# Kernel optimization log

Measured on AMD Instinct MI355X. Metric: run time of the kernel, lower is better.

## Reference

```python
import jax, jax.numpy as jnp
import numpy as np

E, H, W = 1024, 16, 256  # embed_dim, num_heads, window_size
D = E // H               # head_dim


def _rmsnorm(t, w):
    eps = jnp.finfo(t.dtype).eps
    return t * jax.lax.rsqrt(jnp.mean(t * t, axis=-1, keepdims=True) + eps) * w


def setup_inputs() -> dict:
    key = jax.random.key(0)
    ks = jax.random.split(key, 11)
    B, T = 2, 2048
    s = 1.0 / np.sqrt(E)
    return {
        "x": jax.random.normal(ks[0], (B, T, E), jnp.float32),
        "wq": jax.random.normal(ks[1], (E, E), jnp.float32) * s,
        "bq": jnp.zeros((E,), jnp.float32),
        "wk": jax.random.normal(ks[2], (E, E), jnp.float32) * s,
        "bk": jnp.zeros((E,), jnp.float32),
        "wv": jax.random.normal(ks[3], (E, E), jnp.float32) * s,
        "bv": jnp.zeros((E,), jnp.float32),
        "wo": jax.random.normal(ks[4], (E, E), jnp.float32) * s,
        "bo": jnp.zeros((E,), jnp.float32),
        "qn_w": jnp.ones((D,), jnp.float32),
        "kn_w": jnp.ones((D,), jnp.float32),
    }


def reference(x, wq, bq, wk, bk, wv, bv, wo, bo, qn_w, kn_w):
    B, T, _ = x.shape
    # projections; weights stored (in, out)
    q = (x @ wq + bq).reshape(B, T, H, D).transpose(0, 2, 1, 3)  # [B,H,T,D]
    k = (x @ wk + bk).reshape(B, T, H, D).transpose(0, 2, 1, 3)
    v = (x @ wv + bv).reshape(B, T, H, D).transpose(0, 2, 1, 3)
    q = _rmsnorm(q, qn_w)
    k = _rmsnorm(k, kn_w)

    scores = jnp.einsum("bhqd,bhkd->bhqk", q, k) / jnp.sqrt(jnp.float32(D))
    row = jnp.arange(T)[:, None]
    col = jnp.arange(T)[None, :]
    invalid = (col > row) | (row - col >= W)  # causal + sliding window
    neg_inf = jnp.float32(-jnp.inf)
    scores = jnp.where(invalid, neg_inf, scores)

    # genetic fitness reweighting
    masked_attn = jnp.where(invalid, 0.0, jax.nn.softmax(scores, axis=-1))
    gene_means = jnp.mean(jax.nn.sigmoid(masked_attn), axis=-1)  # [B,H,T]
    denom = gene_means + 0.5
    sum_inv = jnp.sum(1.0 / denom, axis=2, keepdims=True)        # [B,H,1]
    fitness = 1.0 / (denom * sum_inv)                            # [B,H,T]
    scores = scores + jnp.log(fitness)[..., None]

    attn = jax.nn.softmax(scores, axis=-1)
    out = jnp.einsum("bhqk,bhkd->bhqd", attn, v)
    out = out.transpose(0, 2, 1, 3).reshape(B, T, E)
    return out @ wo + bo
```

## Files before the change

kernel.cpp:

```cpp
#include <hip/hip_runtime.h>

typedef _Float16 f16;
typedef _Float16 f16x4 __attribute__((ext_vector_type(4)));
typedef _Float16 f16x8 __attribute__((ext_vector_type(8)));
typedef float f32x4 __attribute__((ext_vector_type(4)));

#define MFMA16(a, b, c) __builtin_amdgcn_mfma_f32_16x16x32_f16(a, b, c, 0, 0, 0)

constexpr int T = 2048;
constexpr int E = 1024;
constexpr int H = 16;
constexpr int D = 64;
constexpr int WIN = 256;
#define NEGF (-1e30f)
#define L2E 1.4426950408889634f

__device__ __forceinline__ void gload16(const f16* g, f16* l) {
  __builtin_amdgcn_global_load_lds(
      (__attribute__((address_space(1))) void*)(void*)g,
      (__attribute__((address_space(3))) void*)(void*)l, 16, 0, 0);
}

__global__ __launch_bounds__(256) void cast_x_kernel(const float* __restrict__ x,
                                                     f16* __restrict__ xb) {
  int idx = (blockIdx.x * 256 + threadIdx.x) * 4;
  float4 v = *(const float4*)(x + idx);
  f16x4 o = {(f16)v.x, (f16)v.y, (f16)v.z, (f16)v.w};
  *(f16x4*)(xb + idx) = o;
}

__global__ __launch_bounds__(256) void transpose_w_kernel(
    const float* __restrict__ w0, const float* __restrict__ w1,
    const float* __restrict__ w2, const float* __restrict__ w3,
    f16* __restrict__ o0, f16* __restrict__ o1, f16* __restrict__ o2,
    f16* __restrict__ o3) {
  int z = blockIdx.z;
  const float* w = z == 0 ? w0 : z == 1 ? w1 : z == 2 ? w2 : w3;
  f16* o = z == 0 ? o0 : z == 1 ? o1 : z == 2 ? o2 : o3;
  __shared__ float tile[64][65];
  int k0 = blockIdx.x * 64, n0 = blockIdx.y * 64;
  int r = threadIdx.x >> 2, cb = (threadIdx.x & 3) * 16;
  const float* src = w + (size_t)(k0 + r) * E + n0 + cb;
#pragma unroll
  for (int j = 0; j < 16; j += 4) {
    float4 v = *(const float4*)(src + j);
    tile[r][cb + j] = v.x;
    tile[r][cb + j + 1] = v.y;
    tile[r][cb + j + 2] = v.z;
    tile[r][cb + j + 3] = v.w;
  }
  __syncthreads();
  f16 tmp[16];
#pragma unroll
  for (int j = 0; j < 16; ++j) tmp[j] = (f16)tile[cb + j][r];
  f16* dst = o + (size_t)(n0 + r) * E + k0 + cb;
  *(f16x8*)dst = *(f16x8*)&tmp[0];
  *(f16x8*)(dst + 8) = *(f16x8*)&tmp[8];
}

__global__ __launch_bounds__(256) void qkv_fused_kernel(
    const f16* __restrict__ A, const f16* __restrict__ Bq,
    const f16* __restrict__ Bk, const f16* __restrict__ Bv,
    const float* __restrict__ cq, const float* __restrict__ ck,
    const float* __restrict__ cv, const float* __restrict__ qnw,
    const float* __restrict__ knw, f16* __restrict__ oq, f16* __restrict__ ok,
    f16* __restrict__ Vt) {
  const int K = E, N = E;
  __shared__ f16 lA[2][8192];
  __shared__ f16 lB[3][2][8192];

  int m0 = blockIdx.x * 128, n0 = blockIdx.y * 128;
  int tid = threadIdx.x;
  int wid = tid >> 6, lane = tid & 63;
  int wm = wid >> 1, wn = wid & 1;
  int lr = lane & 15, lg = lane >> 4;

  f32x4 zero = {0.f, 0.f, 0.f, 0.f};
  f32x4 acc[3][4][4];
#pragma unroll
  for (int z = 0; z < 3; ++z)
    for (int a = 0; a < 4; ++a)
      for (int b = 0; b < 4; ++b) acc[z][a][b] = zero;

  int srow = lane >> 3;
  int scol = (lane & 7) << 3;

  auto stage = [&](int buf, int k0) {
#pragma unroll
    for (int p = 0; p < 4; ++p) {
      int cc = (wid << 2) + p;
      int row = (cc << 3) + srow;
      int gc = scol ^ ((row & 7) << 3);
      size_t ga = (size_t)(m0 + row) * K + k0 + gc;
      size_t gb = (size_t)(n0 + row) * K + k0 + gc;
      gload16(A + ga, &lA[buf][cc << 9]);
      gload16(Bq + gb, &lB[0][buf][cc << 9]);
      gload16(Bk + gb, &lB[1][buf][cc << 9]);
      gload16(Bv + gb, &lB[2][buf][cc << 9]);
    }
  };

  stage(0, 0);
  __syncthreads();
  int cur = 0;
  for (int t = 0; t < 16; ++t) {
    if (t + 1 < 16) stage(cur ^ 1, (t + 1) << 6);
#pragma unroll
    for (int kk = 0; kk < 2; ++kk) {
      int kc = kk * 32 + (lg << 3);
      f16x8 af[4];
#pragma unroll
      for (int mt = 0; mt < 4; ++mt) {
        int row = wm * 64 + mt * 16 + lr;
        af[mt] = *(const f16x8*)&lA[cur][((row << 6) + kc) ^ ((row & 7) << 3)];
      }
#pragma unroll
      for (int z = 0; z < 3; ++z) {
#pragma unroll
        for (int nt = 0; nt < 4; ++nt) {
          int row = wn * 64 + nt * 16 + lr;
          f16x8 bf =
              *(const f16x8*)&lB[z][cur][((row << 6) + kc) ^ ((row & 7) << 3)];
#pragma unroll
          for (int mt = 0; mt < 4; ++mt)
            acc[z][mt][nt] = MFMA16(af[mt], bf, acc[z][mt][nt]);
        }
      }
    }
    if (t + 1 < 16) {
      __syncthreads();
      cur ^= 1;
    }
  }

  const float eps = 1.1920929e-7f;
#pragma unroll
  for (int z = 0; z < 2; ++z) {
    const float* nw = z == 0 ? qnw : knw;
    const float* bias = z == 0 ? cq : ck;
    f16* o = z == 0 ? oq : ok;
    const float osc = z == 0 ? 0.125f : 1.0f;
    float wv_[4];
#pragma unroll
    for (int nt = 0; nt < 4; ++nt) wv_[nt] = nw[nt * 16 + lr] * osc;
#pragma unroll
    for (int mt = 0; mt < 4; ++mt) {
      float vbuf[4][4];
      float ss[4] = {0.f, 0.f, 0.f, 0.f};
#pragma unroll
      for (int nt = 0; nt < 4; ++nt) {
        float bv = bias[n0 + wn * 64 + nt * 16 + lr];
#pragma unroll
        for (int i = 0; i < 4; ++i) {
          float v = acc[z][mt][nt][i] + bv;
          vbuf[nt][i] = v;
          ss[i] += v * v;
        }
      }
      float rr[4];
#pragma unroll
      for (int i = 0; i < 4; ++i) {
        ss[i] += __shfl_xor(ss[i], 1);
        ss[i] += __shfl_xor(ss[i], 2);
        ss[i] += __shfl_xor(ss[i], 4);
        ss[i] += __shfl_xor(ss[i], 8);
        rr[i] = rsqrtf(ss[i] * (1.0f / 64.0f) + eps);
      }
      int row = m0 + wm * 64 + mt * 16 + (lg << 2);
#pragma unroll
      for (int nt = 0; nt < 4; ++nt) {
        int col = n0 + wn * 64 + nt * 16 + lr;
#pragma unroll
        for (int i = 0; i < 4; ++i)
          o[(size_t)(row + i) * N + col] = (f16)(vbuf[nt][i] * rr[i] * wv_[nt]);
      }
    }
  }
#pragma unroll
  for (int mt = 0; mt < 4; ++mt) {
    int row = m0 + wm * 64 + mt * 16 + (lg << 2);
    int b = row >> 11;
    int t = row & (T - 1);
#pragma unroll
    for (int nt = 0; nt < 4; ++nt) {
      int col = n0 + wn * 64 + nt * 16 + lr;
      float bv = cv[col];
      int h = col >> 6, d = col & 63;
      f16x4 pk = {(f16)(acc[2][mt][nt][0] + bv), (f16)(acc[2][mt][nt][1] + bv),
                  (f16)(acc[2][mt][nt][2] + bv), (f16)(acc[2][mt][nt][3] + bv)};
      *(f16x4*)&Vt[(((size_t)(b * H + h) * D + d) << 11) + t] = pk;
    }
  }
}

__global__ __launch_bounds__(256) void out_gemm_kernel(
    const f16* __restrict__ A, const f16* __restrict__ Bt,
    const float* __restrict__ bias, float* __restrict__ out, int M, int N,
    int K) {
  __shared__ f16 lA[2][8192];
  __shared__ f16 lB[2][8192];

  int m0 = blockIdx.x * 128, n0 = blockIdx.y * 128;
  int tid = threadIdx.x;
  int wid = tid >> 6, lane = tid & 63;
  int wm = wid >> 1, wn = wid & 1;
  int lr = lane & 15, lg = lane >> 4;

  f32x4 zero = {0.f, 0.f, 0.f, 0.f};
  f32x4 acc[4][4];
  for (int a = 0; a < 4; ++a)
    for (int b = 0; b < 4; ++b) acc[a][b] = zero;

  int srow = lane >> 3;
  int scol = (lane & 7) << 3;

  auto stage = [&](int buf, int k0) {
#pragma unroll
    for (int p = 0; p < 4; ++p) {
      int cc = (wid << 2) + p;
      int row = (cc << 3) + srow;
      int gc = scol ^ ((row & 7) << 3);
      gload16(A + (size_t)(m0 + row) * K + k0 + gc, &lA[buf][cc << 9]);
      gload16(Bt + (size_t)(n0 + row) * K + k0 + gc, &lB[buf][cc << 9]);
    }
  };

  int nit = K >> 6;
  stage(0, 0);
  __syncthreads();
  int cur = 0;
  for (int t = 0; t < nit; ++t) {
    if (t + 1 < nit) stage(cur ^ 1, (t + 1) << 6);
#pragma unroll
    for (int kk = 0; kk < 2; ++kk) {
      int kc = kk * 32 + (lg << 3);
      f16x8 af[4], bf[4];
#pragma unroll
      for (int mt = 0; mt < 4; ++mt) {
        int row = wm * 64 + mt * 16 + lr;
        af[mt] = *(const f16x8*)&lA[cur][((row << 6) + kc) ^ ((row & 7) << 3)];
      }
#pragma unroll
      for (int nt = 0; nt < 4; ++nt) {
        int row = wn * 64 + nt * 16 + lr;
        bf[nt] = *(const f16x8*)&lB[cur][((row << 6) + kc) ^ ((row & 7) << 3)];
      }
#pragma unroll
      for (int mt = 0; mt < 4; ++mt)
#pragma unroll
        for (int nt = 0; nt < 4; ++nt)
          acc[mt][nt] = MFMA16(af[mt], bf[nt], acc[mt][nt]);
    }
    if (t + 1 < nit) {
      __syncthreads();
      cur ^= 1;
    }
  }

#pragma unroll
  for (int mt = 0; mt < 4; ++mt) {
#pragma unroll
    for (int nt = 0; nt < 4; ++nt) {
      int row = m0 + wm * 64 + mt * 16 + (lg << 2);
      int col = n0 + wn * 64 + nt * 16 + lr;
      float bv = bias[col];
#pragma unroll
      for (int i = 0; i < 4; ++i)
        out[(size_t)(row + i) * N + col] = acc[mt][nt][i] + bv;
    }
  }
}

__global__ __launch_bounds__(256) void attn_kernel(const f16* __restrict__ qn,
                                                   const f16* __restrict__ kn,
                                                   const f16* __restrict__ Vt,
                                                   f16* __restrict__ aout) {
  int q0 = blockIdx.x * 64;
  int bh = blockIdx.y;
  int b = bh >> 4, h = bh & 15;
  int tid = threadIdx.x;
  int w = tid >> 6, lane = tid & 63;
  int lr = lane & 15, lg = lane >> 4;

  __shared__ f16 lK[2][4096];
  __shared__ f16 lV[2][4096];
  __shared__ f16 lP[4096];

  const f16* Qb = qn + (size_t)(b * T + q0 + w * 16 + lr) * E + h * 64 + (lg << 3);
  f16x8 qf0 = *(const f16x8*)Qb;
  f16x8 qf1 = *(const f16x8*)(Qb + 32);

  f32x4 zero = {0.f, 0.f, 0.f, 0.f};
  f32x4 acc[4] = {zero, zero, zero, zero};
  float m[4] = {NEGF, NEGF, NEGF, NEGF};
  float l[4] = {0.f, 0.f, 0.f, 0.f};

  int mi = q0 >> 6;
  int kts = mi - 4 < 0 ? 0 : mi - 4;

  const f16* Kbase = kn + (size_t)b * T * E + h * 64;
  const f16* Vbase = Vt + (size_t)bh * D * T;

  int srow = lane >> 3;
  int scol = (lane & 7) << 3;

  auto stageKV = [&](int buf, int kt) {
    int k0 = kt << 6;
#pragma unroll
    for (int p = 0; p < 2; ++p) {
      int cc = (w << 1) + p;
      int row = (cc << 3) + srow;
      int gc = scol ^ ((row & 7) << 3);
      gload16(Kbase + (size_t)(k0 + row) * E + gc, &lK[buf][cc << 9]);
      gload16(Vbase + (size_t)row * T + k0 + gc, &lV[buf][cc << 9]);
    }
  };

  stageKV(0, kts);
  __syncthreads();
  int cur = 0;

  for (int kt = kts; kt <= mi; ++kt) {
    if (kt < mi) stageKV(cur ^ 1, kt + 1);
    int k0 = kt << 6;

    f32x4 s[4];
#pragma unroll
    for (int ct = 0; ct < 4; ++ct) s[ct] = zero;
#pragma unroll
    for (int kk = 0; kk < 2; ++kk) {
      int kc = kk * 32 + (lg << 3);
#pragma unroll
      for (int ct = 0; ct < 4; ++ct) {
        int row = ct * 16 + lr;
        f16x8 bf = *(const f16x8*)&lK[cur][((row << 6) + kc) ^ ((row & 7) << 3)];
        s[ct] = MFMA16(kk == 0 ? qf0 : qf1, bf, s[ct]);
      }
    }

    float tm[4] = {NEGF, NEGF, NEGF, NEGF};
    int rowg0 = q0 + w * 16 + (lg << 2);
    bool needmask = (kt == mi) || (mi >= 4 && kt == kts);
    if (needmask) {
#pragma unroll
      for (int ct = 0; ct < 4; ++ct) {
        int col = k0 + ct * 16 + lr;
#pragma unroll
        for (int i = 0; i < 4; ++i) {
          int rowg = rowg0 + i;
          float v = s[ct][i];
          if (col > rowg || rowg - col >= WIN) v = NEGF;
          s[ct][i] = v;
          tm[i] = fmaxf(tm[i], v);
        }
      }
    } else {
#pragma unroll
      for (int ct = 0; ct < 4; ++ct)
#pragma unroll
        for (int i = 0; i < 4; ++i) tm[i] = fmaxf(tm[i], s[ct][i]);
    }
#pragma unroll
    for (int i = 0; i < 4; ++i) {
      tm[i] = fmaxf(tm[i], __shfl_xor(tm[i], 1));
      tm[i] = fmaxf(tm[i], __shfl_xor(tm[i], 2));
      tm[i] = fmaxf(tm[i], __shfl_xor(tm[i], 4));
      tm[i] = fmaxf(tm[i], __shfl_xor(tm[i], 8));
    }
    bool up = (tm[0] > m[0]) || (tm[1] > m[1]) || (tm[2] > m[2]) ||
              (tm[3] > m[3]);
    if (__any(up)) {
      float fac[4];
#pragma unroll
      for (int i = 0; i < 4; ++i) {
        float mn = fmaxf(m[i], tm[i]);
        fac[i] = exp2f((m[i] - mn) * L2E);
        m[i] = mn;
        l[i] *= fac[i];
      }
#pragma unroll
      for (int dt = 0; dt < 4; ++dt)
#pragma unroll
        for (int i = 0; i < 4; ++i) acc[dt][i] *= fac[i];
    }
    float ps[4] = {0.f, 0.f, 0.f, 0.f};
#pragma unroll
    for (int ct = 0; ct < 4; ++ct)
#pragma unroll
      for (int i = 0; i < 4; ++i) {
        float p = exp2f((s[ct][i] - m[i]) * L2E);
        s[ct][i] = p;
        ps[i] += p;
      }
#pragma unroll
    for (int i = 0; i < 4; ++i) {
      ps[i] += __shfl_xor(ps[i], 1);
      ps[i] += __shfl_xor(ps[i], 2);
      ps[i] += __shfl_xor(ps[i], 4);
      ps[i] += __shfl_xor(ps[i], 8);
      l[i] += ps[i];
    }

#pragma unroll
    for (int ct = 0; ct < 4; ++ct)
#pragma unroll
      for (int i = 0; i < 4; ++i) {
        int qloc = (lg << 2) + i;
        int el = (qloc << 6) + ct * 16 + lr;
        lP[w * 1024 + (el ^ ((qloc & 7) << 3))] = (f16)s[ct][i];
      }

#pragma unroll
    for (int kk = 0; kk < 2; ++kk) {
      int kc = kk * 32 + (lg << 3);
      int ep = w * 1024 + (((lr << 6) + kc) ^ ((lr & 7) << 3));
      f16x8 pf = *(const f16x8*)&lP[ep];
#pragma unroll
      for (int dt = 0; dt < 4; ++dt) {
        int row = dt * 16 + lr;
        f16x8 vf = *(const f16x8*)&lV[cur][((row << 6) + kc) ^ ((row & 7) << 3)];
        acc[dt] = MFMA16(pf, vf, acc[dt]);
      }
    }

    if (kt < mi) {
      __syncthreads();
      cur ^= 1;
    }
  }

#pragma unroll
  for (int i = 0; i < 4; ++i) {
    float inv = 1.0f / l[i];
    int tok = q0 + w * 16 + (lg << 2) + i;
    f16* dst = aout + (size_t)(b * T + tok) * E + h * 64 + lr;
#pragma unroll
    for (int dt = 0; dt < 4; ++dt) dst[dt * 16] = (f16)(acc[dt][i] * inv);
  }
}

extern "C" void kernel_launch(void* const* d_in, const int* in_sizes, int n_in,
                              void* d_out, int out_size, void* d_ws,
                              size_t ws_size, hipStream_t stream) {
  const float* x = (const float*)d_in[0];
  const float* wq = (const float*)d_in[1];
  const float* bq = (const float*)d_in[2];
  const float* wk = (const float*)d_in[3];
  const float* bk = (const float*)d_in[4];
  const float* wv = (const float*)d_in[5];
  const float* bv = (const float*)d_in[6];
  const float* wo = (const float*)d_in[7];
  const float* bo = (const float*)d_in[8];
  const float* qn_w = (const float*)d_in[9];
  const float* kn_w = (const float*)d_in[10];
  float* out = (float*)d_out;

  char* ws = (char*)d_ws;
  const size_t MB = 1u << 20;
  f16* xb = (f16*)(ws);
  f16* wqT = (f16*)(ws + 8 * MB);
  f16* wkT = (f16*)(ws + 10 * MB);
  f16* wvT = (f16*)(ws + 12 * MB);
  f16* woT = (f16*)(ws + 14 * MB);
  f16* qn = (f16*)(ws + 16 * MB);
  f16* kn = (f16*)(ws + 24 * MB);
  f16* Vt = (f16*)(ws + 32 * MB);
  f16* aout = (f16*)(ws + 40 * MB);

  cast_x_kernel<<<4096, 256, 0, stream>>>(x, xb);
  transpose_w_kernel<<<dim3(16, 16, 4), 256, 0, stream>>>(wq, wk, wv, wo, wqT,
                                                          wkT, wvT, woT);
  qkv_fused_kernel<<<dim3(32, 8), 256, 0, stream>>>(
      xb, wqT, wkT, wvT, bq, bk, bv, qn_w, kn_w, qn, kn, Vt);
  attn_kernel<<<dim3(32, 32), 256, 0, stream>>>(qn, kn, Vt, aout);
  out_gemm_kernel<<<dim3(32, 8), 256, 0, stream>>>(aout, woT, bo, out, 4096,
                                                   1024, 1024);
}
```

Baseline: 107.7 us.

## Restructure QKV GEMM into 256x256 tiles over concatenated weights with split-phase pipeline

Replaces the fused QKV kernel, which computed q, k and v for a 128x128 tile, with a 512-thread kernel that computes one 256x256 output tile of the concatenated QKV weight matrix. Each block now produces only q, k or v, and the grid becomes 16x12 (192 blocks) instead of 256. The K loop is split into two half-steps with staggered A/B loads, manual waitcnt and barriers, and setprio around the MFMA bursts, so that loads overlap with compute. This aims to raise arithmetic intensity per LDS byte and cut pipeline stalls, at the cost of fewer blocks than CUs and more register pressure.

```diff
diff --git a/kernel.cpp b/kernel.cpp
--- a/kernel.cpp
+++ b/kernel.cpp
@@ -58,84 +58,120 @@
   *(f16x8*)(dst + 8) = *(f16x8*)&tmp[8];
 }
 
-__global__ __launch_bounds__(256) void qkv_fused_kernel(
-    const f16* __restrict__ A, const f16* __restrict__ Bq,
-    const f16* __restrict__ Bk, const f16* __restrict__ Bv,
+__global__ __launch_bounds__(512) void qkv256_kernel(
+    const f16* __restrict__ A, const f16* __restrict__ Ball,
     const float* __restrict__ cq, const float* __restrict__ ck,
     const float* __restrict__ cv, const float* __restrict__ qnw,
     const float* __restrict__ knw, f16* __restrict__ oq, f16* __restrict__ ok,
     f16* __restrict__ Vt) {
-  const int K = E, N = E;
-  __shared__ f16 lA[2][8192];
-  __shared__ f16 lB[3][2][8192];
-
-  int m0 = blockIdx.x * 128, n0 = blockIdx.y * 128;
+  const int K = E;
+  __shared__ f16 lA[2][16384];
+  __shared__ f16 lB[2][16384];
+
+  int m0 = blockIdx.x * 256;
+  int nb = blockIdx.y;
+  int n0 = nb * 256;
   int tid = threadIdx.x;
   int wid = tid >> 6, lane = tid & 63;
-  int wm = wid >> 1, wn = wid & 1;
+  int wm = wid >> 2, wn = wid & 3;
   int lr = lane & 15, lg = lane >> 4;
 
   f32x4 zero = {0.f, 0.f, 0.f, 0.f};
-  f32x4 acc[3][4][4];
-#pragma unroll
-  for (int z = 0; z < 3; ++z)
-    for (int a = 0; a < 4; ++a)
-      for (int b = 0; b < 4; ++b) acc[z][a][b] = zero;
-
-  int srow = lane >> 3;
-  int scol = (lane & 7) << 3;
-
-  auto stage = [&](int buf, int k0) {
-#pragma unroll
-    for (int p = 0; p < 4; ++p) {
-      int cc = (wid << 2) + p;
-      int row = (cc << 3) + srow;
-      int gc = scol ^ ((row & 7) << 3);
-      size_t ga = (size_t)(m0 + row) * K + k0 + gc;
-      size_t gb = (size_t)(n0 + row) * K + k0 + gc;
-      gload16(A + ga, &lA[buf][cc << 9]);
-      gload16(Bq + gb, &lB[0][buf][cc << 9]);
-      gload16(Bk + gb, &lB[1][buf][cc << 9]);
-      gload16(Bv + gb, &lB[2][buf][cc << 9]);
+  f32x4 acc[8][4];
+#pragma unroll
+  for (int a = 0; a < 8; ++a)
+#pragma unroll
+    for (int b = 0; b < 4; ++b) acc[a][b] = zero;
+
+  int s8 = lane >> 3;
+  int c8 = (lane & 7) << 3;
+
+  auto stageA = [&](int t, int buf) {
+#pragma unroll
+    for (int c = 0; c < 4; ++c) {
+      int row = (c << 6) + (wid << 3) + s8;
+      int gc = c8 ^ ((row & 7) << 3);
+      gload16(A + (size_t)(m0 + row) * K + (t << 6) + gc,
+              &lA[buf][((c << 6) + (wid << 3)) << 6]);
     }
   };
-
-  stage(0, 0);
-  __syncthreads();
-  int cur = 0;
+  auto stageB = [&](int t, int buf) {
+#pragma unroll
+    for (int c = 0; c < 4; ++c) {
+      int row = (c << 6) + (wid << 3) + s8;
+      int gc = c8 ^ ((row & 7) << 3);
+      gload16(Ball + (size_t)(n0 + row) * K + (t << 6) + gc,
+              &lB[buf][((c << 6) + (wid << 3)) << 6]);
+    }
+  };
+
+  stageA(0, 0);
+  stageB(0, 0);
+  stageA(1, 1);
+  asm volatile("s_waitcnt vmcnt(4)" ::: "memory");
+  __builtin_amdgcn_s_barrier();
+  __builtin_amdgcn_sched_barrier(0);
+
   for (int t = 0; t < 16; ++t) {
-    if (t + 1 < 16) stage(cur ^ 1, (t + 1) << 6);
-#pragma unroll
-    for (int kk = 0; kk < 2; ++kk) {
-      int kc = kk * 32 + (lg << 3);
-      f16x8 af[4];
-#pragma unroll
-      for (int mt = 0; mt < 4; ++mt) {
-        int row = wm * 64 + mt * 16 + lr;
-        af[mt] = *(const f16x8*)&lA[cur][((row << 6) + kc) ^ ((row & 7) << 3)];
-      }
-#pragma unroll
-      for (int z = 0; z < 3; ++z) {
-#pragma unroll
-        for (int nt = 0; nt < 4; ++nt) {
-          int row = wn * 64 + nt * 16 + lr;
-          f16x8 bf =
-              *(const f16x8*)&lB[z][cur][((row << 6) + kc) ^ ((row & 7) << 3)];
-#pragma unroll
-          for (int mt = 0; mt < 4; ++mt)
-            acc[z][mt][nt] = MFMA16(af[mt], bf, acc[z][mt][nt]);
-        }
-      }
-    }
+    int buf = t & 1;
+    if (t + 1 < 16) stageB(t + 1, buf ^ 1);
+    f16x8 a0[8], b0[4], a1[8], b1[4];
+#pragma unroll
+    for (int mt = 0; mt < 8; ++mt) {
+      int row = wm * 128 + mt * 16 + lr;
+      a0[mt] =
+          *(const f16x8*)&lA[buf][((row << 6) + (lg << 3)) ^ ((row & 7) << 3)];
+    }
+#pragma unroll
+    for (int nt = 0; nt < 4; ++nt) {
+      int row = wn * 64 + nt * 16 + lr;
+      b0[nt] =
+          *(const f16x8*)&lB[buf][((row << 6) + (lg << 3)) ^ ((row & 7) << 3)];
+    }
+#pragma unroll
+    for (int mt = 0; mt < 8; ++mt) {
+      int row = wm * 128 + mt * 16 + lr;
+      a1[mt] = *(const f16x8*)&lA[buf][((row << 6) + 32 + (lg << 3)) ^
+                                       ((row & 7) << 3)];
+    }
+#pragma unroll
+    for (int nt = 0; nt < 4; ++nt) {
+      int row = wn * 64 + nt * 16 + lr;
+      b1[nt] = *(const f16x8*)&lB[buf][((row << 6) + 32 + (lg << 3)) ^
+                                       ((row & 7) << 3)];
+    }
+    __builtin_amdgcn_s_setprio(1);
+#pragma unroll
+    for (int mt = 0; mt < 8; ++mt)
+#pragma unroll
+      for (int nt = 0; nt < 4; ++nt)
+        acc[mt][nt] = MFMA16(a0[mt], b0[nt], acc[mt][nt]);
+    __builtin_amdgcn_s_setprio(0);
+    asm volatile("s_waitcnt lgkmcnt(0)" ::: "memory");
+    __builtin_amdgcn_sched_barrier(0);
+    __builtin_amdgcn_s_barrier();
+    if (t + 2 < 16) stageA(t + 2, buf);
+    __builtin_amdgcn_s_setprio(1);
+#pragma unroll
+    for (int mt = 0; mt < 8; ++mt)
+#pragma unroll
+      for (int nt = 0; nt < 4; ++nt)
+        acc[mt][nt] = MFMA16(a1[mt], b1[nt], acc[mt][nt]);
+    __builtin_amdgcn_s_setprio(0);
     if (t + 1 < 16) {
-      __syncthreads();
-      cur ^= 1;
-    }
-  }
-
+      if (t + 2 < 16)
+        asm volatile("s_waitcnt vmcnt(4)" ::: "memory");
+      else
+        asm volatile("s_waitcnt vmcnt(0)" ::: "memory");
+      __builtin_amdgcn_s_barrier();
+      __builtin_amdgcn_sched_barrier(0);
+    }
+  }
+
+  int z = nb >> 2;
+  int n0z = (nb & 3) * 256;
   const float eps = 1.1920929e-7f;
-#pragma unroll
-  for (int z = 0; z < 2; ++z) {
+  if (z < 2) {
     const float* nw = z == 0 ? qnw : knw;
     const float* bias = z == 0 ? cq : ck;
     f16* o = z == 0 ? oq : ok;
@@ -144,15 +180,15 @@
 #pragma unroll
     for (int nt = 0; nt < 4; ++nt) wv_[nt] = nw[nt * 16 + lr] * osc;
 #pragma unroll
-    for (int mt = 0; mt < 4; ++mt) {
+    for (int mt = 0; mt < 8; ++mt) {
       float vbuf[4][4];
       float ss[4] = {0.f, 0.f, 0.f, 0.f};
 #pragma unroll
       for (int nt = 0; nt < 4; ++nt) {
-        float bv = bias[n0 + wn * 64 + nt * 16 + lr];
+        float bv = bias[n0z + wn * 64 + nt * 16 + lr];
 #pragma unroll
         for (int i = 0; i < 4; ++i) {
-          float v = acc[z][mt][nt][i] + bv;
+          float v = acc[mt][nt][i] + bv;
           vbuf[nt][i] = v;
           ss[i] += v * v;
         }
@@ -166,29 +202,30 @@
         ss[i] += __shfl_xor(ss[i], 8);
         rr[i] = rsqrtf(ss[i] * (1.0f / 64.0f) + eps);
       }
-      int row = m0 + wm * 64 + mt * 16 + (lg << 2);
+      int row = m0 + wm * 128 + mt * 16 + (lg << 2);
 #pragma unroll
       for (int nt = 0; nt < 4; ++nt) {
-        int col = n0 + wn * 64 + nt * 16 + lr;
+        int col = n0z + wn * 64 + nt * 16 + lr;
 #pragma unroll
         for (int i = 0; i < 4; ++i)
-          o[(size_t)(row + i) * N + col] = (f16)(vbuf[nt][i] * rr[i] * wv_[nt]);
-      }
-    }
-  }
-#pragma unroll
-  for (int mt = 0; mt < 4; ++mt) {
-    int row = m0 + wm * 64 + mt * 16 + (lg << 2);
-    int b = row >> 11;
-    int t = row & (T - 1);
-#pragma unroll
-    for (int nt = 0; nt < 4; ++nt) {
-      int col = n0 + wn * 64 + nt * 16 + lr;
-      float bv = cv[col];
-      int h = col >> 6, d = col & 63;
-      f16x4 pk = {(f16)(acc[2][mt][nt][0] + bv), (f16)(acc[2][mt][nt][1] + bv),
-                  (f16)(acc[2][mt][nt][2] + bv), (f16)(acc[2][mt][nt][3] + bv)};
-      *(f16x4*)&Vt[(((size_t)(b * H + h) * D + d) << 11) + t] = pk;
+          o[(size_t)(row + i) * E + col] = (f16)(vbuf[nt][i] * rr[i] * wv_[nt]);
+      }
+    }
+  } else {
+#pragma unroll
+    for (int mt = 0; mt < 8; ++mt) {
+      int row = m0 + wm * 128 + mt * 16 + (lg << 2);
+      int b = row >> 11;
+      int tt = row & (T - 1);
+#pragma unroll
+      for (int nt = 0; nt < 4; ++nt) {
+        int col = n0z + wn * 64 + nt * 16 + lr;
+        float bv = cv[col];
+        int h = col >> 6, d = col & 63;
+        f16x4 pk = {(f16)(acc[mt][nt][0] + bv), (f16)(acc[mt][nt][1] + bv),
+                    (f16)(acc[mt][nt][2] + bv), (f16)(acc[mt][nt][3] + bv)};
+        *(f16x4*)&Vt[(((size_t)(b * H + h) * D + d) << 11) + tt] = pk;
+      }
     }
   }
 }
@@ -458,9 +495,10 @@
   char* ws = (char*)d_ws;
   const size_t MB = 1u << 20;
   f16* xb = (f16*)(ws);
-  f16* wqT = (f16*)(ws + 8 * MB);
-  f16* wkT = (f16*)(ws + 10 * MB);
-  f16* wvT = (f16*)(ws + 12 * MB);
+  f16* wAll = (f16*)(ws + 8 * MB);
+  f16* wqT = wAll;
+  f16* wkT = wAll + (size_t)E * E;
+  f16* wvT = wAll + 2 * (size_t)E * E;
   f16* woT = (f16*)(ws + 14 * MB);
   f16* qn = (f16*)(ws + 16 * MB);
   f16* kn = (f16*)(ws + 24 * MB);
@@ -470,8 +508,8 @@
   cast_x_kernel<<<4096, 256, 0, stream>>>(x, xb);
   transpose_w_kernel<<<dim3(16, 16, 4), 256, 0, stream>>>(wq, wk, wv, wo, wqT,
                                                           wkT, wvT, woT);
-  qkv_fused_kernel<<<dim3(32, 8), 256, 0, stream>>>(
-      xb, wqT, wkT, wvT, bq, bk, bv, qn_w, kn_w, qn, kn, Vt);
+  qkv256_kernel<<<dim3(16, 12), 512, 0, stream>>>(xb, wAll, bq, bk, bv, qn_w,
+                                                  kn_w, qn, kn, Vt);
   attn_kernel<<<dim3(32, 32), 256, 0, stream>>>(qn, kn, Vt, aout);
   out_gemm_kernel<<<dim3(32, 8), 256, 0, stream>>>(aout, woT, bo, out, 4096,
                                                    1024, 1024);
```

Result: slower. 115.1 us (+7.0%).
